# Kernel tuning notes

Measured on AMD Instinct MI355X. Metric: run time of the kernel, lower is better.

## Reference

```python
import jax, jax.numpy as jnp
import numpy as np
from jax.scipy.special import logsumexp

B, T, H, L = 64, 512, 768, 9


def setup_inputs() -> dict:
    key = jax.random.key(0)
    ks = jax.random.split(key, 8)
    length = jax.random.randint(ks[0], (B,), 0, T, dtype=jnp.int32)
    word2vec = jax.random.normal(ks[1], (B, T, H), dtype=jnp.float32)
    mask = jnp.ones((B, T), dtype=jnp.int32)
    label = jax.random.randint(ks[2], (B, T), 0, L, dtype=jnp.int32)
    # Linear(768 -> num_labels) params (PyTorch default init scale)
    bound = 1.0 / np.sqrt(H)
    W = jax.random.uniform(ks[3], (L, H), jnp.float32, -bound, bound)
    b = jax.random.uniform(ks[4], (L,), jnp.float32, -bound, bound)
    # CRF params (torchcrf init: uniform(-0.1, 0.1))
    start_transitions = jax.random.uniform(ks[5], (L,), jnp.float32, -0.1, 0.1)
    end_transitions = jax.random.uniform(ks[6], (L,), jnp.float32, -0.1, 0.1)
    transitions = jax.random.uniform(ks[7], (L, L), jnp.float32, -0.1, 0.1)
    return {"length": length, "word2vec": word2vec, "mask": mask, "label": label,
            "W": W, "b": b, "start_transitions": start_transitions,
            "end_transitions": end_transitions, "transitions": transitions}


def _crf_nll(emissions, tags, mask, start_transitions, end_transitions, transitions):
    # emissions [B,T,L], tags [B,T] int, mask [B,T] {0,1}
    Bn, Tn, Ln = emissions.shape
    maskf = mask.astype(emissions.dtype)
    # ---- numerator: score of the given tag sequence ----
    batch = jnp.arange(Bn)
    score = start_transitions[tags[:, 0]] + emissions[batch, 0, tags[:, 0]]
    # transition scores for steps 1..T-1, vectorized over time
    trans_sc = transitions[tags[:, :-1], tags[:, 1:]]                    # [B,T-1]
    emit_sc = jnp.take_along_axis(emissions, tags[..., None], axis=2)[..., 0]  # [B,T]
    score = score + jnp.sum((trans_sc + emit_sc[:, 1:]) * maskf[:, 1:], axis=1)
    seq_ends = jnp.sum(mask, axis=1).astype(jnp.int32) - 1
    last_tags = tags[batch, seq_ends]
    numerator = score + end_transitions[last_tags]
    # ---- denominator: log partition via forward algorithm (scan over time) ----
    em_t = jnp.transpose(emissions, (1, 0, 2))   # [T,B,L]
    mk_t = jnp.transpose(mask, (1, 0)) != 0      # [T,B]
    alpha0 = start_transitions[None, :] + em_t[0]  # [B,L]

    def step(alpha, inp):
        em_i, m_i = inp
        # alpha[b, i] + transitions[i, j] + emissions[b, j]
        nxt = logsumexp(alpha[:, :, None] + transitions[None, :, :] + em_i[:, None, :], axis=1)
        alpha = jnp.where(m_i[:, None], nxt, alpha)
        return alpha, None

    alpha, _ = jax.lax.scan(step, alpha0, (em_t[1:], mk_t[1:]))
    denominator = logsumexp(alpha + end_transitions[None, :], axis=1)
    llh = numerator - denominator
    return -jnp.mean(llh)


def reference(length, word2vec, mask, label, W, b, start_transitions, end_transitions, transitions):
    # dropout p=0.0 -> identity; Linear projection to emissions
    emissions = jnp.einsum('bth,lh->btl', word2vec, W) + b  # [B,T,L]
    return _crf_nll(emissions, label, mask, start_transitions, end_transitions, transitions)
```

## Files before the change

### kernel.cpp

```cpp
#include <hip/hip_runtime.h>
#include <hip/hip_bf16.h>


#define Bn 64
#define Tn 512
#define Hn 768
#define Ln 9
#define EMS 12
#define CS 16
#define NCH 32
#define KSTEPS 24

typedef short bf16x8 __attribute__((ext_vector_type(8)));
typedef float f32x4  __attribute__((ext_vector_type(4)));

__device__ __forceinline__ short f2bf(float f) {
    return (short)__builtin_bit_cast(unsigned short, __float2bfloat16(f));
}

__global__ __launch_bounds__(256) void emis_kernel(
    const float* __restrict__ wv, const float* __restrict__ Wm,
    const float* __restrict__ bias, float* __restrict__ eexp, int* __restrict__ cnt)
{
    if (blockIdx.x == 0 && threadIdx.x == 0) cnt[0] = 0;

    __shared__ bf16x8 wlds[KSTEPS * 64];

    for (int idx = threadIdx.x; idx < KSTEPS * 64; idx += 256) {
        const int kk = idx >> 6, ln = idx & 63;
        const int n = ln & 15, kb = ln >> 4;
        bf16x8 v;
        if (n < Ln) {
            const float* src = Wm + n * Hn + kk * 32 + kb * 8;
#pragma unroll
            for (int j = 0; j < 8; ++j) v[j] = f2bf(src[j]);
        } else {
#pragma unroll
            for (int j = 0; j < 8; ++j) v[j] = 0;
        }
        wlds[idx] = v;
    }
    __syncthreads();

    const int lane = threadIdx.x & 63;
    const int tile = (blockIdx.x << 2) + (threadIdx.x >> 6);
    const int m    = lane & 15;
    const int kb   = lane >> 4;
    const float* abase = wv + (size_t)(tile * 16 + m) * Hn + kb * 8;

    f32x4 acc = {0.f, 0.f, 0.f, 0.f};
#pragma unroll 4
    for (int kk = 0; kk < KSTEPS; ++kk) {
        float4 x0 = *reinterpret_cast<const float4*>(abase + kk * 32);
        float4 x1 = *reinterpret_cast<const float4*>(abase + kk * 32 + 4);
        bf16x8 a;
        a[0] = f2bf(x0.x); a[1] = f2bf(x0.y); a[2] = f2bf(x0.z); a[3] = f2bf(x0.w);
        a[4] = f2bf(x1.x); a[5] = f2bf(x1.y); a[6] = f2bf(x1.z); a[7] = f2bf(x1.w);
        bf16x8 b = wlds[kk * 64 + lane];
        acc = __builtin_amdgcn_mfma_f32_16x16x32_bf16(a, b, acc, 0, 0, 0);
    }

    const int l = lane & 15;
    if (l < Ln) {
        const float bl = bias[l];
#pragma unroll
        for (int r = 0; r < 4; ++r) {
            const int row = tile * 16 + (lane >> 4) * 4 + r;
            eexp[(size_t)row * EMS + l] = __expf(acc[r] + bl);
        }
    }
}

__global__ __launch_bounds__(320) void fwd_kernel(
    const float* __restrict__ eexp, const int* __restrict__ mask,
    const int* __restrict__ label, const float* __restrict__ trans,
    const float* __restrict__ startT, const float* __restrict__ endT,
    float* __restrict__ partial, int* __restrict__ cnt, float* __restrict__ out)
{
    __shared__ float sM[NCH][Ln][Ln];
    __shared__ float sLg[NCH][Ln];
    __shared__ float sM2[NCH / 2][Ln][Ln];
    __shared__ float sLg2[NCH / 2][Ln];
    __shared__ float eTs[81];
    __shared__ float sp[5];
    __shared__ int   si[5];

    const int b    = blockIdx.x;
    const int tid  = threadIdx.x;
    const int lane = tid & 63;
    const int wid  = tid >> 6;

    if (tid < 81) eTs[tid] = __expf(trans[tid]);

    float part = 0.f; int msum = 0;
    for (int t = tid; t < Tn; t += 320) {
        int tag = label[b * Tn + t];
        int mk  = mask[b * Tn + t];
        msum += mk;
        if (t == 0) {
            part += startT[tag] + __logf(eexp[(size_t)(b * Tn) * EMS + tag]);
        } else if (mk) {
            int prev = label[b * Tn + t - 1];
            part += trans[prev * Ln + tag] + __logf(eexp[(size_t)(b * Tn + t) * EMS + tag]);
        }
    }
#pragma unroll
    for (int off = 32; off > 0; off >>= 1) {
        part += __shfl_xor(part, off);
        msum += __shfl_xor(msum, off);
    }
    if (lane == 0) { sp[wid] = part; si[wid] = msum; }

    __syncthreads();

    if (tid < NCH * Ln) {
        float Tr[81];
#pragma unroll
        for (int i = 0; i < 81; ++i) Tr[i] = eTs[i];
        const int r = tid % Ln;
        const int c = tid / Ln;

        float v[9];
#pragma unroll
        for (int k = 0; k < 9; ++k) v[k] = (k == r) ? 1.f : 0.f;
        float lg = 0.f;

        const int t0 = 1 + c * CS;
        const int t1 = min(Tn, t0 + CS);
        const float* eb = eexp + (size_t)(b * Tn) * EMS;
        const int* mrow = mask + b * Tn;

        float4 e0 = *reinterpret_cast<const float4*>(eb + t0 * EMS);
        float4 e1 = *reinterpret_cast<const float4*>(eb + t0 * EMS + 4);
        float  e8 = eb[t0 * EMS + 8];
        int    mk = mrow[t0];

        for (int t = t0; t < t1; ++t) {
            float4 p0 = make_float4(0.f, 0.f, 0.f, 0.f), p1 = p0;
            float  p8 = 0.f; int pm = 0;
            if (t + 1 < t1) {
                p0 = *reinterpret_cast<const float4*>(eb + (t + 1) * EMS);
                p1 = *reinterpret_cast<const float4*>(eb + (t + 1) * EMS + 4);
                p8 = eb[(t + 1) * EMS + 8];
                pm = mrow[t + 1];
            }
            if (mk) {
                float e[9] = {e0.x, e0.y, e0.z, e0.w, e1.x, e1.y, e1.z, e1.w, e8};
                float nv[9];
#pragma unroll
                for (int jj = 0; jj < 9; ++jj) {
                    float acc = v[0] * Tr[jj];
#pragma unroll
                    for (int k = 1; k < 9; ++k) acc += v[k] * Tr[k * 9 + jj];
                    nv[jj] = acc * e[jj];
                }
                float mx = nv[0];
#pragma unroll
                for (int jj = 1; jj < 9; ++jj) mx = fmaxf(mx, nv[jj]);
                float inv = 1.f / mx;
#pragma unroll
                for (int jj = 0; jj < 9; ++jj) v[jj] = nv[jj] * inv;
                lg += __logf(mx);
            }
            e0 = p0; e1 = p1; e8 = p8; mk = pm;
        }
#pragma unroll
        for (int jj = 0; jj < 9; ++jj) sM[c][r][jj] = v[jj];
        sLg[c][r] = lg;
    }
    __syncthreads();

    if (tid < (NCH / 2) * Ln) {
        const int r = tid % Ln;
        const int p = tid / Ln;
        float mB = sLg[2 * p + 1][0];
#pragma unroll
        for (int k = 1; k < 9; ++k) mB = fmaxf(mB, sLg[2 * p + 1][k]);
        float tA[9];
#pragma unroll
        for (int k = 0; k < 9; ++k) tA[k] = sM[2 * p][r][k] * __expf(sLg[2 * p + 1][k] - mB);
        float v[9];
#pragma unroll
        for (int jj = 0; jj < 9; ++jj) {
            float acc = tA[0] * sM[2 * p + 1][0][jj];
#pragma unroll
            for (int k = 1; k < 9; ++k) acc += tA[k] * sM[2 * p + 1][k][jj];
            v[jj] = acc;
        }
        float mx = v[0];
#pragma unroll
        for (int jj = 1; jj < 9; ++jj) mx = fmaxf(mx, v[jj]);
        float inv = 1.f / mx;
#pragma unroll
        for (int jj = 0; jj < 9; ++jj) sM2[p][r][jj] = v[jj] * inv;
        sLg2[p][r] = sLg[2 * p][r] + mB + __logf(mx);
    }
    __syncthreads();

    if (tid < 16) {
        const int lj = tid;
        const float NEG = -1e30f;
        float la = (lj < Ln) ? (startT[lj] + __logf(eexp[(size_t)(b * Tn) * EMS + lj])) : NEG;
        for (int c = 0; c < NCH / 2; ++c) {
            float mc[9];
#pragma unroll
            for (int rr = 0; rr < 9; ++rr) mc[rr] = (lj < Ln) ? sM2[c][rr][lj] : 0.f;
            float x = (lj < Ln) ? (la + sLg2[c][lj]) : NEG;
            float mm = x;
#pragma unroll
            for (int off = 1; off < 16; off <<= 1) mm = fmaxf(mm, __shfl_xor(mm, off, 16));
            float w = __expf(x - mm);
            float sacc = 0.f;
#pragma unroll
            for (int rr = 0; rr < 9; ++rr) sacc += __shfl(w, rr, 16) * mc[rr];
            la = (lj < Ln) ? (mm + __logf(sacc)) : NEG;
        }
        float x = (lj < Ln) ? (la + endT[lj]) : NEG;
        float mm = x;
#pragma unroll
        for (int off = 1; off < 16; off <<= 1) mm = fmaxf(mm, __shfl_xor(mm, off, 16));
        float se = __expf(x - mm);
#pragma unroll
        for (int off = 1; off < 16; off <<= 1) se += __shfl_xor(se, off, 16);
        if (lj == 0) {
            float denom = mm + __logf(se);
            float numer = sp[0] + sp[1] + sp[2] + sp[3] + sp[4];
            int   sm    = si[0] + si[1] + si[2] + si[3] + si[4];
            int   last  = label[b * Tn + sm - 1];
            partial[b]  = denom - (numer + endT[last]);
        }
    }

    if (tid < 64) {
        int old = 0;
        if (tid == 0) {
            __threadfence();
            old = atomicAdd(cnt, 1);
        }
        old = __shfl(old, 0);
        if (old == Bn - 1) {
            __threadfence();
            float pv = partial[tid];
#pragma unroll
            for (int off = 32; off > 0; off >>= 1) pv += __shfl_xor(pv, off);
            if (tid == 0) out[0] = pv * (1.0f / Bn);
        }
    }
}

extern "C" void kernel_launch(void* const* d_in, const int* in_sizes, int n_in,
                              void* d_out, int out_size, void* d_ws, size_t ws_size,
                              hipStream_t stream)
{
    const float* wv    = (const float*)d_in[1];
    const int*   mask  = (const int*)d_in[2];
    const int*   label = (const int*)d_in[3];
    const float* Wm    = (const float*)d_in[4];
    const float* bias  = (const float*)d_in[5];
    const float* st    = (const float*)d_in[6];
    const float* en    = (const float*)d_in[7];
    const float* tr    = (const float*)d_in[8];

    float* ws      = (float*)d_ws;
    float* eexp    = ws;
    float* partial = ws + 393216;
    int*   cnt     = (int*)(ws + 393280);
    float* out     = (float*)d_out;

    hipLaunchKernelGGL(emis_kernel, dim3(512), dim3(256), 0, stream,
                       wv, Wm, bias, eexp, cnt);
    hipLaunchKernelGGL(fwd_kernel, dim3(Bn), dim3(320), 0, stream,
                       eexp, mask, label, tr, st, en, partial, cnt, out);
}
```

Measured before the change: 48.51 us.

## Fuse emission GEMM and CRF forward into one kernel via last-block-per-batch

Merges the emission projection kernel and the CRF forward kernel into a single 512-block launch. Each block computes its emission tiles, then atomically increments a per-batch counter, and the eighth block to finish for a batch runs the forward algorithm for it. Shared memory is reused between the weight tile and the forward-pass buffers. This removes the inter-kernel gap and lets forward work start while other batches are still in the GEMM. In exchange it adds a memset launch and fence/atomic overhead, and the serial forward pass now runs in whichever block finishes last for each batch.

```diff
diff --git a/kernel.cpp b/kernel.cpp
--- a/kernel.cpp
+++ b/kernel.cpp
@@ -18,77 +18,83 @@
     return (short)__builtin_bit_cast(unsigned short, __float2bfloat16(f));
 }
 
-__global__ __launch_bounds__(256) void emis_kernel(
+__global__ __launch_bounds__(320) void fused_kernel(
     const float* __restrict__ wv, const float* __restrict__ Wm,
-    const float* __restrict__ bias, float* __restrict__ eexp, int* __restrict__ cnt)
-{
-    if (blockIdx.x == 0 && threadIdx.x == 0) cnt[0] = 0;
-
-    __shared__ bf16x8 wlds[KSTEPS * 64];
-
-    for (int idx = threadIdx.x; idx < KSTEPS * 64; idx += 256) {
-        const int kk = idx >> 6, ln = idx & 63;
-        const int n = ln & 15, kb = ln >> 4;
-        bf16x8 v;
-        if (n < Ln) {
-            const float* src = Wm + n * Hn + kk * 32 + kb * 8;
-#pragma unroll
-            for (int j = 0; j < 8; ++j) v[j] = f2bf(src[j]);
-        } else {
-#pragma unroll
-            for (int j = 0; j < 8; ++j) v[j] = 0;
-        }
-        wlds[idx] = v;
-    }
-    __syncthreads();
-
-    const int lane = threadIdx.x & 63;
-    const int tile = (blockIdx.x << 2) + (threadIdx.x >> 6);
-    const int m    = lane & 15;
-    const int kb   = lane >> 4;
-    const float* abase = wv + (size_t)(tile * 16 + m) * Hn + kb * 8;
-
-    f32x4 acc = {0.f, 0.f, 0.f, 0.f};
-#pragma unroll 4
-    for (int kk = 0; kk < KSTEPS; ++kk) {
-        float4 x0 = *reinterpret_cast<const float4*>(abase + kk * 32);
-        float4 x1 = *reinterpret_cast<const float4*>(abase + kk * 32 + 4);
-        bf16x8 a;
-        a[0] = f2bf(x0.x); a[1] = f2bf(x0.y); a[2] = f2bf(x0.z); a[3] = f2bf(x0.w);
-        a[4] = f2bf(x1.x); a[5] = f2bf(x1.y); a[6] = f2bf(x1.z); a[7] = f2bf(x1.w);
-        bf16x8 b = wlds[kk * 64 + lane];
-        acc = __builtin_amdgcn_mfma_f32_16x16x32_bf16(a, b, acc, 0, 0, 0);
-    }
-
-    const int l = lane & 15;
-    if (l < Ln) {
-        const float bl = bias[l];
-#pragma unroll
-        for (int r = 0; r < 4; ++r) {
-            const int row = tile * 16 + (lane >> 4) * 4 + r;
-            eexp[(size_t)row * EMS + l] = __expf(acc[r] + bl);
-        }
-    }
-}
-
-__global__ __launch_bounds__(320) void fwd_kernel(
-    const float* __restrict__ eexp, const int* __restrict__ mask,
+    const float* __restrict__ bias, const int* __restrict__ mask,
     const int* __restrict__ label, const float* __restrict__ trans,
     const float* __restrict__ startT, const float* __restrict__ endT,
-    float* __restrict__ partial, int* __restrict__ cnt, float* __restrict__ out)
+    float* __restrict__ eexp, float* __restrict__ partial,
+    int* __restrict__ bcnt, int* __restrict__ cnt2,
+    float* __restrict__ out)
 {
-    __shared__ float sM[NCH][Ln][Ln];
-    __shared__ float sLg[NCH][Ln];
-    __shared__ float sM2[NCH / 2][Ln][Ln];
-    __shared__ float sLg2[NCH / 2][Ln];
-    __shared__ float eTs[81];
+    __shared__ __align__(16) char smraw[24576];
     __shared__ float sp[5];
     __shared__ int   si[5];
-
-    const int b    = blockIdx.x;
+    __shared__ int   sFlag;
+
     const int tid  = threadIdx.x;
     const int lane = tid & 63;
     const int wid  = tid >> 6;
+
+    bf16x8* wlds = reinterpret_cast<bf16x8*>(smraw);
+    for (int idx = tid; idx < KSTEPS * 64; idx += 320) {
+        const int kk = idx >> 6, ln = idx & 63;
+        const int n = ln & 15, kb2 = ln >> 4;
+        bf16x8 v;
+        if (n < Ln) {
+            const float* src = Wm + n * Hn + kk * 32 + kb2 * 8;
+#pragma unroll
+            for (int j = 0; j < 8; ++j) v[j] = f2bf(src[j]);
+        } else {
+#pragma unroll
+            for (int j = 0; j < 8; ++j) v[j] = 0;
+        }
+        wlds[idx] = v;
+    }
+    __syncthreads();
+
+    if (wid < 4) {
+        const int tile = (blockIdx.x << 2) + wid;
+        const int m    = lane & 15;
+        const int kb   = lane >> 4;
+        const float* abase = wv + (size_t)(tile * 16 + m) * Hn + kb * 8;
+
+        f32x4 acc = {0.f, 0.f, 0.f, 0.f};
+#pragma unroll 4
+        for (int kk = 0; kk < KSTEPS; ++kk) {
+            float4 x0 = *reinterpret_cast<const float4*>(abase + kk * 32);
+            float4 x1 = *reinterpret_cast<const float4*>(abase + kk * 32 + 4);
+            bf16x8 a;
+            a[0] = f2bf(x0.x); a[1] = f2bf(x0.y); a[2] = f2bf(x0.z); a[3] = f2bf(x0.w);
+            a[4] = f2bf(x1.x); a[5] = f2bf(x1.y); a[6] = f2bf(x1.z); a[7] = f2bf(x1.w);
+            bf16x8 bfr = wlds[kk * 64 + lane];
+            acc = __builtin_amdgcn_mfma_f32_16x16x32_bf16(a, bfr, acc, 0, 0, 0);
+        }
+
+        const int l = lane & 15;
+        if (l < Ln) {
+            const float bl = bias[l];
+#pragma unroll
+            for (int r = 0; r < 4; ++r) {
+                const int row = tile * 16 + (lane >> 4) * 4 + r;
+                eexp[(size_t)row * EMS + l] = __expf(acc[r] + bl);
+            }
+        }
+    }
+
+    __threadfence();
+    __syncthreads();
+    const int b = blockIdx.x >> 3;
+    if (tid == 0) sFlag = (atomicAdd(&bcnt[b], 1) == 7);
+    __syncthreads();
+    if (!sFlag) return;
+    __threadfence();
+
+    float (*sM)[Ln][Ln]  = reinterpret_cast<float(*)[Ln][Ln]>(smraw);
+    float (*sLg)[Ln]     = reinterpret_cast<float(*)[Ln]>(smraw + 10368);
+    float (*sM2)[Ln][Ln] = reinterpret_cast<float(*)[Ln][Ln]>(smraw + 11520);
+    float (*sLg2)[Ln]    = reinterpret_cast<float(*)[Ln]>(smraw + 16704);
+    float* eTs           = reinterpret_cast<float*>(smraw + 17280);
 
     if (tid < 81) eTs[tid] = __expf(trans[tid]);
 
@@ -235,7 +241,7 @@
         int old = 0;
         if (tid == 0) {
             __threadfence();
-            old = atomicAdd(cnt, 1);
+            old = atomicAdd(cnt2, 1);
         }
         old = __shfl(old, 0);
         if (old == Bn - 1) {
@@ -264,11 +270,13 @@
     float* ws      = (float*)d_ws;
     float* eexp    = ws;
     float* partial = ws + 393216;
-    int*   cnt     = (int*)(ws + 393280);
+    int*   bcnt    = (int*)(ws + 393280);
+    int*   cnt2    = bcnt + Bn;
     float* out     = (float*)d_out;
 
-    hipLaunchKernelGGL(emis_kernel, dim3(512), dim3(256), 0, stream,
-                       wv, Wm, bias, eexp, cnt);
-    hipLaunchKernelGGL(fwd_kernel, dim3(Bn), dim3(320), 0, stream,
-                       eexp, mask, label, tr, st, en, partial, cnt, out);
+    hipMemsetAsync(bcnt, 0, (Bn + 1) * sizeof(int), stream);
+
+    hipLaunchKernelGGL(fused_kernel, dim3(512), dim3(320), 0, stream,
+                       wv, Wm, bias, mask, label, tr, st, en,
+                       eexp, partial, bcnt, cnt2, out);
 }
```

After: 153.2 us. +215.8%, slower.

## Fuse emission GEMM with per-quarter CRF chunk products in shared memory

Applied to the files above, without the earlier changes.

The emission projection and the chunked forward-algorithm matrix products are merged into one kernel. Each block handles a 128-step quarter of one sequence, keeps its exp-emissions in LDS instead of writing them to global memory, and tree-reduces its chunk transfer matrices down to one 9x9 matrix per quarter. A small second kernel then chains the four quarter matrices per sequence and performs the final mean reduction. This removes the global round trip of the emission tensor and spreads the serial scan across 256 blocks instead of 64. The cost is larger blocks with more LDS and extra barriers.

```diff
diff --git a/kernel.cpp b/kernel.cpp
--- a/kernel.cpp
+++ b/kernel.cpp
@@ -8,7 +8,8 @@
 #define Ln 9
 #define EMS 12
 #define CS 16
-#define NCH 32
+#define NCHQ 8
+#define QT 128
 #define KSTEPS 24
 
 typedef short bf16x8 __attribute__((ext_vector_type(8)));
@@ -18,20 +19,41 @@
     return (short)__builtin_bit_cast(unsigned short, __float2bfloat16(f));
 }
 
-__global__ __launch_bounds__(256) void emis_kernel(
+__global__ __launch_bounds__(512) void emis_q_kernel(
     const float* __restrict__ wv, const float* __restrict__ Wm,
-    const float* __restrict__ bias, float* __restrict__ eexp, int* __restrict__ cnt)
+    const float* __restrict__ bias, const int* __restrict__ mask,
+    const int* __restrict__ label, const float* __restrict__ trans,
+    const float* __restrict__ startT,
+    float* __restrict__ Mq, float* __restrict__ lgq,
+    float* __restrict__ numq, int* __restrict__ msq,
+    float* __restrict__ em0, int* __restrict__ cnt)
 {
-    if (blockIdx.x == 0 && threadIdx.x == 0) cnt[0] = 0;
-
     __shared__ bf16x8 wlds[KSTEPS * 64];
-
-    for (int idx = threadIdx.x; idx < KSTEPS * 64; idx += 256) {
+    __shared__ float  ldsE[QT][EMS];
+    __shared__ int    ldsM[QT];
+    __shared__ float  eTs[81];
+    __shared__ float  sM[NCHQ][Ln][Ln];
+    __shared__ float  sLg[NCHQ][Ln];
+    __shared__ float  sp[8];
+    __shared__ int    si[8];
+
+    const int tid   = threadIdx.x;
+    const int lane  = tid & 63;
+    const int wid   = tid >> 6;
+    const int bid   = blockIdx.x;
+    const int b     = bid >> 2;
+    const int q     = bid & 3;
+    const int tbase = q * QT;
+
+    if (bid == 0 && tid == 0) cnt[0] = 0;
+    if (tid < 81) eTs[tid] = __expf(trans[tid]);
+
+    for (int idx = tid; idx < KSTEPS * 64; idx += 512) {
         const int kk = idx >> 6, ln = idx & 63;
-        const int n = ln & 15, kb = ln >> 4;
+        const int n = ln & 15, kb2 = ln >> 4;
         bf16x8 v;
         if (n < Ln) {
-            const float* src = Wm + n * Hn + kk * 32 + kb * 8;
+            const float* src = Wm + n * Hn + kk * 32 + kb2 * 8;
 #pragma unroll
             for (int j = 0; j < 8; ++j) v[j] = f2bf(src[j]);
         } else {
@@ -42,78 +64,56 @@
     }
     __syncthreads();
 
-    const int lane = threadIdx.x & 63;
-    const int tile = (blockIdx.x << 2) + (threadIdx.x >> 6);
-    const int m    = lane & 15;
-    const int kb   = lane >> 4;
-    const float* abase = wv + (size_t)(tile * 16 + m) * Hn + kb * 8;
-
-    f32x4 acc = {0.f, 0.f, 0.f, 0.f};
+    {
+        const int m  = lane & 15;
+        const int kb = lane >> 4;
+        const float* abase = wv + (size_t)(bid * QT + wid * 16 + m) * Hn + kb * 8;
+
+        f32x4 acc = {0.f, 0.f, 0.f, 0.f};
 #pragma unroll 4
-    for (int kk = 0; kk < KSTEPS; ++kk) {
-        float4 x0 = *reinterpret_cast<const float4*>(abase + kk * 32);
-        float4 x1 = *reinterpret_cast<const float4*>(abase + kk * 32 + 4);
-        bf16x8 a;
-        a[0] = f2bf(x0.x); a[1] = f2bf(x0.y); a[2] = f2bf(x0.z); a[3] = f2bf(x0.w);
-        a[4] = f2bf(x1.x); a[5] = f2bf(x1.y); a[6] = f2bf(x1.z); a[7] = f2bf(x1.w);
-        bf16x8 b = wlds[kk * 64 + lane];
-        acc = __builtin_amdgcn_mfma_f32_16x16x32_bf16(a, b, acc, 0, 0, 0);
-    }
-
-    const int l = lane & 15;
-    if (l < Ln) {
-        const float bl = bias[l];
-#pragma unroll
-        for (int r = 0; r < 4; ++r) {
-            const int row = tile * 16 + (lane >> 4) * 4 + r;
-            eexp[(size_t)row * EMS + l] = __expf(acc[r] + bl);
-        }
-    }
-}
-
-__global__ __launch_bounds__(320) void fwd_kernel(
-    const float* __restrict__ eexp, const int* __restrict__ mask,
-    const int* __restrict__ label, const float* __restrict__ trans,
-    const float* __restrict__ startT, const float* __restrict__ endT,
-    float* __restrict__ partial, int* __restrict__ cnt, float* __restrict__ out)
-{
-    __shared__ float sM[NCH][Ln][Ln];
-    __shared__ float sLg[NCH][Ln];
-    __shared__ float sM2[NCH / 2][Ln][Ln];
-    __shared__ float sLg2[NCH / 2][Ln];
-    __shared__ float eTs[81];
-    __shared__ float sp[5];
-    __shared__ int   si[5];
-
-    const int b    = blockIdx.x;
-    const int tid  = threadIdx.x;
-    const int lane = tid & 63;
-    const int wid  = tid >> 6;
-
-    if (tid < 81) eTs[tid] = __expf(trans[tid]);
-
-    float part = 0.f; int msum = 0;
-    for (int t = tid; t < Tn; t += 320) {
-        int tag = label[b * Tn + t];
-        int mk  = mask[b * Tn + t];
-        msum += mk;
-        if (t == 0) {
-            part += startT[tag] + __logf(eexp[(size_t)(b * Tn) * EMS + tag]);
+        for (int kk = 0; kk < KSTEPS; ++kk) {
+            float4 x0 = *reinterpret_cast<const float4*>(abase + kk * 32);
+            float4 x1 = *reinterpret_cast<const float4*>(abase + kk * 32 + 4);
+            bf16x8 a;
+            a[0] = f2bf(x0.x); a[1] = f2bf(x0.y); a[2] = f2bf(x0.z); a[3] = f2bf(x0.w);
+            a[4] = f2bf(x1.x); a[5] = f2bf(x1.y); a[6] = f2bf(x1.z); a[7] = f2bf(x1.w);
+            bf16x8 bfr = wlds[kk * 64 + lane];
+            acc = __builtin_amdgcn_mfma_f32_16x16x32_bf16(a, bfr, acc, 0, 0, 0);
+        }
+        const int l = lane & 15;
+        if (l < Ln) {
+            const float bl = bias[l];
+#pragma unroll
+            for (int r = 0; r < 4; ++r) {
+                const int lrow = wid * 16 + (lane >> 4) * 4 + r;
+                ldsE[lrow][l] = __expf(acc[r] + bl);
+            }
+        }
+    }
+    __syncthreads();
+
+    float part = 0.f; int ms = 0;
+    if (tid < QT) {
+        const int gt  = tbase + tid;
+        const int tag = label[b * Tn + gt];
+        const int mk  = mask[b * Tn + gt];
+        ldsM[tid] = mk; ms = mk;
+        if (gt == 0) {
+            part = startT[tag] + __logf(ldsE[0][tag]);
         } else if (mk) {
-            int prev = label[b * Tn + t - 1];
-            part += trans[prev * Ln + tag] + __logf(eexp[(size_t)(b * Tn + t) * EMS + tag]);
+            const int prev = label[b * Tn + gt - 1];
+            part = trans[prev * Ln + tag] + __logf(ldsE[tid][tag]);
         }
     }
 #pragma unroll
     for (int off = 32; off > 0; off >>= 1) {
         part += __shfl_xor(part, off);
-        msum += __shfl_xor(msum, off);
-    }
-    if (lane == 0) { sp[wid] = part; si[wid] = msum; }
-
-    __syncthreads();
-
-    if (tid < NCH * Ln) {
+        ms   += __shfl_xor(ms, off);
+    }
+    if (lane == 0) { sp[wid] = part; si[wid] = ms; }
+    __syncthreads();
+
+    if (tid < NCHQ * Ln) {
         float Tr[81];
 #pragma unroll
         for (int i = 0; i < 81; ++i) Tr[i] = eTs[i];
@@ -125,27 +125,27 @@
         for (int k = 0; k < 9; ++k) v[k] = (k == r) ? 1.f : 0.f;
         float lg = 0.f;
 
-        const int t0 = 1 + c * CS;
-        const int t1 = min(Tn, t0 + CS);
-        const float* eb = eexp + (size_t)(b * Tn) * EMS;
-        const int* mrow = mask + b * Tn;
-
-        float4 e0 = *reinterpret_cast<const float4*>(eb + t0 * EMS);
-        float4 e1 = *reinterpret_cast<const float4*>(eb + t0 * EMS + 4);
-        float  e8 = eb[t0 * EMS + 8];
-        int    mk = mrow[t0];
+        int t0 = tbase + c * CS; if (t0 == 0) t0 = 1;
+        const int t1 = tbase + (c + 1) * CS;
+
+        int lt = t0 - tbase;
+        float4 e0v = *reinterpret_cast<const float4*>(&ldsE[lt][0]);
+        float4 e1v = *reinterpret_cast<const float4*>(&ldsE[lt][4]);
+        float  e8  = ldsE[lt][8];
+        int    mk  = ldsM[lt];
 
         for (int t = t0; t < t1; ++t) {
             float4 p0 = make_float4(0.f, 0.f, 0.f, 0.f), p1 = p0;
             float  p8 = 0.f; int pm = 0;
             if (t + 1 < t1) {
-                p0 = *reinterpret_cast<const float4*>(eb + (t + 1) * EMS);
-                p1 = *reinterpret_cast<const float4*>(eb + (t + 1) * EMS + 4);
-                p8 = eb[(t + 1) * EMS + 8];
-                pm = mrow[t + 1];
+                const int nlt = t + 1 - tbase;
+                p0 = *reinterpret_cast<const float4*>(&ldsE[nlt][0]);
+                p1 = *reinterpret_cast<const float4*>(&ldsE[nlt][4]);
+                p8 = ldsE[nlt][8];
+                pm = ldsM[nlt];
             }
             if (mk) {
-                float e[9] = {e0.x, e0.y, e0.z, e0.w, e1.x, e1.y, e1.z, e1.w, e8};
+                float e[9] = {e0v.x, e0v.y, e0v.z, e0v.w, e1v.x, e1v.y, e1v.z, e1v.w, e8};
                 float nv[9];
 #pragma unroll
                 for (int jj = 0; jj < 9; ++jj) {
@@ -162,29 +162,71 @@
                 for (int jj = 0; jj < 9; ++jj) v[jj] = nv[jj] * inv;
                 lg += __logf(mx);
             }
-            e0 = p0; e1 = p1; e8 = p8; mk = pm;
+            e0v = p0; e1v = p1; e8 = p8; mk = pm;
         }
 #pragma unroll
         for (int jj = 0; jj < 9; ++jj) sM[c][r][jj] = v[jj];
         sLg[c][r] = lg;
     }
-    __syncthreads();
-
-    if (tid < (NCH / 2) * Ln) {
-        const int r = tid % Ln;
-        const int p = tid / Ln;
-        float mB = sLg[2 * p + 1][0];
-#pragma unroll
-        for (int k = 1; k < 9; ++k) mB = fmaxf(mB, sLg[2 * p + 1][k]);
+    if (q == 0 && tid >= 72 && tid < 81) em0[b * Ln + (tid - 72)] = ldsE[0][tid - 72];
+    if (tid == 100) {
+        float s = 0.f; int m2 = 0;
+#pragma unroll
+        for (int i = 0; i < 8; ++i) { s += sp[i]; m2 += si[i]; }
+        numq[bid] = s; msq[bid] = m2;
+    }
+    __syncthreads();
+
+    for (int n = 4; n >= 2; n >>= 1) {
+        float vout[9]; float lgout = 0.f;
+        const bool act = tid < n * Ln;
+        int p = 0, r = 0;
+        if (act) {
+            p = tid / Ln; r = tid % Ln;
+            float mB = sLg[2 * p + 1][0];
+#pragma unroll
+            for (int k = 1; k < 9; ++k) mB = fmaxf(mB, sLg[2 * p + 1][k]);
+            float tA[9];
+#pragma unroll
+            for (int k = 0; k < 9; ++k) tA[k] = sM[2 * p][r][k] * __expf(sLg[2 * p + 1][k] - mB);
+#pragma unroll
+            for (int jj = 0; jj < 9; ++jj) {
+                float acc = tA[0] * sM[2 * p + 1][0][jj];
+#pragma unroll
+                for (int k = 1; k < 9; ++k) acc += tA[k] * sM[2 * p + 1][k][jj];
+                vout[jj] = acc;
+            }
+            float mx = vout[0];
+#pragma unroll
+            for (int jj = 1; jj < 9; ++jj) mx = fmaxf(mx, vout[jj]);
+            float inv = 1.f / mx;
+#pragma unroll
+            for (int jj = 0; jj < 9; ++jj) vout[jj] *= inv;
+            lgout = sLg[2 * p][r] + mB + __logf(mx);
+        }
+        __syncthreads();
+        if (act) {
+#pragma unroll
+            for (int jj = 0; jj < 9; ++jj) sM[p][r][jj] = vout[jj];
+            sLg[p][r] = lgout;
+        }
+        __syncthreads();
+    }
+
+    if (tid < Ln) {
+        const int r = tid;
+        float mB = sLg[1][0];
+#pragma unroll
+        for (int k = 1; k < 9; ++k) mB = fmaxf(mB, sLg[1][k]);
         float tA[9];
 #pragma unroll
-        for (int k = 0; k < 9; ++k) tA[k] = sM[2 * p][r][k] * __expf(sLg[2 * p + 1][k] - mB);
+        for (int k = 0; k < 9; ++k) tA[k] = sM[0][r][k] * __expf(sLg[1][k] - mB);
         float v[9];
 #pragma unroll
         for (int jj = 0; jj < 9; ++jj) {
-            float acc = tA[0] * sM[2 * p + 1][0][jj];
-#pragma unroll
-            for (int k = 1; k < 9; ++k) acc += tA[k] * sM[2 * p + 1][k][jj];
+            float acc = tA[0] * sM[1][0][jj];
+#pragma unroll
+            for (int k = 1; k < 9; ++k) acc += tA[k] * sM[1][k][jj];
             v[jj] = acc;
         }
         float mx = v[0];
@@ -192,20 +234,41 @@
         for (int jj = 1; jj < 9; ++jj) mx = fmaxf(mx, v[jj]);
         float inv = 1.f / mx;
 #pragma unroll
-        for (int jj = 0; jj < 9; ++jj) sM2[p][r][jj] = v[jj] * inv;
-        sLg2[p][r] = sLg[2 * p][r] + mB + __logf(mx);
-    }
+        for (int jj = 0; jj < 9; ++jj) Mq[bid * 81 + r * 9 + jj] = v[jj] * inv;
+        lgq[bid * Ln + r] = sLg[0][r] + mB + __logf(mx);
+    }
+}
+
+__global__ __launch_bounds__(64) void comb_kernel(
+    const float* __restrict__ Mq, const float* __restrict__ lgq,
+    const float* __restrict__ numq, const int* __restrict__ msq,
+    const float* __restrict__ em0, const int* __restrict__ label,
+    const float* __restrict__ startT, const float* __restrict__ endT,
+    float* __restrict__ partial, int* __restrict__ cnt, float* __restrict__ out)
+{
+    __shared__ float cM[4][Ln][Ln];
+    __shared__ float cLg[4][Ln];
+    __shared__ float cem[Ln];
+    __shared__ float cnum[4];
+    __shared__ int   cms[4];
+
+    const int b = blockIdx.x, tid = threadIdx.x;
+
+    for (int i = tid; i < 4 * 81; i += 64) cM[i / 81][(i % 81) / 9][i % 9] = Mq[b * 324 + i];
+    for (int i = tid; i < 4 * 9; i += 64)  cLg[i / 9][i % 9] = lgq[b * 36 + i];
+    if (tid < Ln) cem[tid] = em0[b * Ln + tid];
+    if (tid < 4) { cnum[tid] = numq[b * 4 + tid]; cms[tid] = msq[b * 4 + tid]; }
     __syncthreads();
 
     if (tid < 16) {
         const int lj = tid;
         const float NEG = -1e30f;
-        float la = (lj < Ln) ? (startT[lj] + __logf(eexp[(size_t)(b * Tn) * EMS + lj])) : NEG;
-        for (int c = 0; c < NCH / 2; ++c) {
+        float la = (lj < Ln) ? (startT[lj] + __logf(cem[lj])) : NEG;
+        for (int c = 0; c < 4; ++c) {
             float mc[9];
 #pragma unroll
-            for (int rr = 0; rr < 9; ++rr) mc[rr] = (lj < Ln) ? sM2[c][rr][lj] : 0.f;
-            float x = (lj < Ln) ? (la + sLg2[c][lj]) : NEG;
+            for (int rr = 0; rr < 9; ++rr) mc[rr] = (lj < Ln) ? cM[c][rr][lj] : 0.f;
+            float x = (lj < Ln) ? (la + cLg[c][lj]) : NEG;
             float mm = x;
 #pragma unroll
             for (int off = 1; off < 16; off <<= 1) mm = fmaxf(mm, __shfl_xor(mm, off, 16));
@@ -224,27 +287,25 @@
         for (int off = 1; off < 16; off <<= 1) se += __shfl_xor(se, off, 16);
         if (lj == 0) {
             float denom = mm + __logf(se);
-            float numer = sp[0] + sp[1] + sp[2] + sp[3] + sp[4];
-            int   sm    = si[0] + si[1] + si[2] + si[3] + si[4];
+            float numer = cnum[0] + cnum[1] + cnum[2] + cnum[3];
+            int   sm    = cms[0] + cms[1] + cms[2] + cms[3];
             int   last  = label[b * Tn + sm - 1];
             partial[b]  = denom - (numer + endT[last]);
         }
     }
 
-    if (tid < 64) {
-        int old = 0;
-        if (tid == 0) {
-            __threadfence();
-            old = atomicAdd(cnt, 1);
-        }
-        old = __shfl(old, 0);
-        if (old == Bn - 1) {
-            __threadfence();
-            float pv = partial[tid];
-#pragma unroll
-            for (int off = 32; off > 0; off >>= 1) pv += __shfl_xor(pv, off);
-            if (tid == 0) out[0] = pv * (1.0f / Bn);
-        }
+    int old = 0;
+    if (tid == 0) {
+        __threadfence();
+        old = atomicAdd(cnt, 1);
+    }
+    old = __shfl(old, 0);
+    if (old == Bn - 1) {
+        __threadfence();
+        float pv = partial[tid];
+#pragma unroll
+        for (int off = 32; off > 0; off >>= 1) pv += __shfl_xor(pv, off);
+        if (tid == 0) out[0] = pv * (1.0f / Bn);
     }
 }
 
@@ -262,13 +323,19 @@
     const float* tr    = (const float*)d_in[8];
 
     float* ws      = (float*)d_ws;
-    float* eexp    = ws;
-    float* partial = ws + 393216;
-    int*   cnt     = (int*)(ws + 393280);
+    float* Mq      = ws;
+    float* lgq     = ws + 20736;
+    float* numq    = ws + 23040;
+    int*   msq     = (int*)(ws + 23296);
+    float* em0     = ws + 23552;
+    float* partial = ws + 24128;
+    int*   cnt     = (int*)(ws + 24192);
     float* out     = (float*)d_out;
 
-    hipLaunchKernelGGL(emis_kernel, dim3(512), dim3(256), 0, stream,
-                       wv, Wm, bias, eexp, cnt);
-    hipLaunchKernelGGL(fwd_kernel, dim3(Bn), dim3(320), 0, stream,
-                       eexp, mask, label, tr, st, en, partial, cnt, out);
+    hipLaunchKernelGGL(emis_q_kernel, dim3(256), dim3(512), 0, stream,
+                       wv, Wm, bias, mask, label, tr, st,
+                       Mq, lgq, numq, msq, em0, cnt);
+    hipLaunchKernelGGL(comb_kernel, dim3(Bn), dim3(64), 0, stream,
+                       Mq, lgq, numq, msq, em0, label, st, en,
+                       partial, cnt, out);
 }
```

Result: faster. 40.07 us (-17.4%).
